# Performance work log

Measured on AMD Instinct MI355X. Metric: run time of the kernel, lower is better.

## Reference

```python
import jax, jax.numpy as jnp
import numpy as np

HIDDEN = 7168
NUM_EXPERTS = 256
TOPK = 8
NUM_GROUPS = 8
TOPK_GROUPS = 4
ROUTE_SCALE = 2.5
TOKENS = 8192


def setup_inputs() -> dict:
    key = jax.random.key(0)
    kx, kw = jax.random.split(key)
    x = jax.random.normal(kx, (TOKENS, HIDDEN), dtype=jnp.float32)
    # gate weight ~ nn.Parameter(empty) initialized here with small normal values
    weight = jax.random.normal(kw, (NUM_EXPERTS, HIDDEN), dtype=jnp.float32) * 0.02
    # bias branch is active because hidden_size == 7168
    bias = jnp.zeros((NUM_EXPERTS,), dtype=jnp.float32)
    return {"x": x, "weight": weight, "bias": bias}


def reference(x, weight, bias):
    # scores: [T, E] = sigmoid(x @ W^T)
    scores = jax.nn.sigmoid(jnp.einsum("th,eh->te", x.astype(jnp.float32), weight))
    original_scores = scores
    scores_for_choice = scores + bias  # bias is not None (hidden==7168)

    T = scores.shape[0]
    per_group = NUM_EXPERTS // NUM_GROUPS  # 32
    g = scores_for_choice.reshape(T, NUM_GROUPS, per_group)
    # bias is not None -> group score = sum of top-2 within each group
    group_scores = jax.lax.top_k(g, 2)[0].sum(axis=-1)  # [T, G]
    _, group_idx = jax.lax.top_k(group_scores, TOPK_GROUPS)  # [T, topk_groups]
    # keep-mask over groups
    keep = jnp.zeros((T, NUM_GROUPS), dtype=bool)
    keep = keep.at[jnp.arange(T)[:, None], group_idx].set(True)
    masked = jnp.where(keep[:, :, None], g, -jnp.inf).reshape(T, NUM_EXPERTS)

    _, indices = jax.lax.top_k(masked, TOPK)  # [T, topk]
    weights = jnp.take_along_axis(original_scores, indices, axis=1)
    weights = weights / (weights.sum(axis=-1, keepdims=True) + 1e-20)
    weights = weights * ROUTE_SCALE
    return weights.astype(jnp.float32), indices
```

## Files before the change

kernel.cpp:

```cpp
#include <hip/hip_runtime.h>
#include <math.h>


constexpr int T_TOK = 8192;
constexpr int HID   = 7168;
constexpr int NEXP  = 256;

constexpr int BM   = 64;
constexpr int BK   = 64;
constexpr int KSPL = 8;
constexpr int KH   = HID / KSPL;
constexpr int NIT  = KH / BK;

typedef __attribute__((ext_vector_type(8)))  _Float16 hf8;
typedef __attribute__((ext_vector_type(4)))  _Float16 hf4;
typedef __attribute__((ext_vector_type(16))) float    f32x16;

struct hl16 { _Float16 h, l; };
__device__ __forceinline__ hl16 cvt_split(float v, float scale) {
  const float s = v * scale;
  const _Float16 h = (_Float16)s;
  const _Float16 l = (_Float16)(s - (float)h);
  return {h, l};
}

__global__ __launch_bounds__(256)
void convert_w(const float* __restrict__ w, _Float16* __restrict__ wh,
               _Float16* __restrict__ wl) {
  const int gid = blockIdx.x * 256 + threadIdx.x;
  const int e = gid / (HID / 4);
  const int c = gid - e * (HID / 4);
  const float4 v = *(const float4*)(w + (size_t)gid * 4);
  const int k = 4 * c;
  const size_t o = (size_t)(k >> 3) * (NEXP * 8) + (size_t)e * 8 + (k & 7);
  hf4 h, l;
  hl16 t;
  t = cvt_split(v.x, 1024.f); h.x = t.h; l.x = t.l;
  t = cvt_split(v.y, 1024.f); h.y = t.h; l.y = t.l;
  t = cvt_split(v.z, 1024.f); h.z = t.h; l.z = t.l;
  t = cvt_split(v.w, 1024.f); h.w = t.h; l.w = t.l;
  *(hf4*)(wh + o) = h;
  *(hf4*)(wl + o) = l;
}

__global__ __launch_bounds__(512, 4)
void gemm_mfma(const float* __restrict__ x, const _Float16* __restrict__ wh,
               const _Float16* __restrict__ wl, float* __restrict__ part) {
  __shared__ __attribute__((aligned(16))) _Float16 Ah[2][BM * BK];
  __shared__ __attribute__((aligned(16))) _Float16 Al[2][BM * BK];

  const int tid = threadIdx.x;
  const int l   = tid & 63;
  const int wn  = tid >> 6;

  const int b  = blockIdx.x;
  const int kp = b & 7;
  const int t0 = (b >> 3) * BM;
  const int kb = kp * KH;

  const int sr = tid >> 3;
  const int sc = tid & 7;
  const float* xrow = x + (size_t)(t0 + sr) * HID + kb + 4 * sc;

  const int swz   = (l & 7) << 4;
  const int lrow  = l & 31;
  const int khalf = l >> 5;

  const _Float16* bhb = wh + ((size_t)(kb >> 3) + khalf) * (NEXP * 8)
                           + (size_t)(wn * 32 + lrow) * 8;
  const _Float16* blb = wl + ((size_t)(kb >> 3) + khalf) * (NEXP * 8)
                           + (size_t)(wn * 32 + lrow) * 8;

  f32x16 acc[2] = {};

  float4 xv0 = *(const float4*)(xrow);
  float4 xv1 = *(const float4*)(xrow + 32);

#pragma unroll 2
  for (int it = 0; it < NIT; ++it) {
    float4 xn0, xn1;
    const bool more = (it + 1 < NIT);
    if (more) {
      xn0 = *(const float4*)(xrow + (it + 1) * BK);
      xn1 = *(const float4*)(xrow + (it + 1) * BK + 32);
    }

    hf8 bh[4], bl[4];
    const _Float16* bhi = bhb + (size_t)it * (8 * NEXP * 8);
    const _Float16* bli = blb + (size_t)it * (8 * NEXP * 8);
#pragma unroll
    for (int ks = 0; ks < 4; ++ks) {
      bh[ks] = *(const hf8*)(bhi + ks * (2 * NEXP * 8));
      bl[ks] = *(const hf8*)(bli + ks * (2 * NEXP * 8));
    }

    _Float16* ah = &Ah[it & 1][0];
    _Float16* al = &Al[it & 1][0];
    {
      hf4 h0, h1, g0, g1;
      hl16 t;
      t = cvt_split(xv0.x, 64.f); h0.x = t.h; g0.x = t.l;
      t = cvt_split(xv0.y, 64.f); h0.y = t.h; g0.y = t.l;
      t = cvt_split(xv0.z, 64.f); h0.z = t.h; g0.z = t.l;
      t = cvt_split(xv0.w, 64.f); h0.w = t.h; g0.w = t.l;
      t = cvt_split(xv1.x, 64.f); h1.x = t.h; g1.x = t.l;
      t = cvt_split(xv1.y, 64.f); h1.y = t.h; g1.y = t.l;
      t = cvt_split(xv1.z, 64.f); h1.z = t.h; g1.z = t.l;
      t = cvt_split(xv1.w, 64.f); h1.w = t.h; g1.w = t.l;
      const int wb  = sr * (BK * 2);
      const int wsw = (sr & 7) << 4;
      *(hf4*)((char*)ah + wb + ((sc * 8)      ^ wsw)) = h0;
      *(hf4*)((char*)ah + wb + ((sc * 8 + 64) ^ wsw)) = h1;
      *(hf4*)((char*)al + wb + ((sc * 8)      ^ wsw)) = g0;
      *(hf4*)((char*)al + wb + ((sc * 8 + 64) ^ wsw)) = g1;
    }

    asm volatile("s_waitcnt lgkmcnt(0)\n\ts_barrier" ::: "memory");

#pragma unroll
    for (int ks = 0; ks < 4; ++ks) {
      const int cb = (ks * 32 + khalf * 16) ^ swz;
      const hf8 a0h = *(const hf8*)((const char*)ah + lrow * 128 + cb);
      const hf8 a1h = *(const hf8*)((const char*)ah + (32 + lrow) * 128 + cb);
      const hf8 a0l = *(const hf8*)((const char*)al + lrow * 128 + cb);
      const hf8 a1l = *(const hf8*)((const char*)al + (32 + lrow) * 128 + cb);
      acc[0] = __builtin_amdgcn_mfma_f32_32x32x16_f16(a0h, bh[ks], acc[0], 0, 0, 0);
      acc[1] = __builtin_amdgcn_mfma_f32_32x32x16_f16(a1h, bh[ks], acc[1], 0, 0, 0);
      acc[0] = __builtin_amdgcn_mfma_f32_32x32x16_f16(a0l, bh[ks], acc[0], 0, 0, 0);
      acc[1] = __builtin_amdgcn_mfma_f32_32x32x16_f16(a1l, bh[ks], acc[1], 0, 0, 0);
      acc[0] = __builtin_amdgcn_mfma_f32_32x32x16_f16(a0h, bl[ks], acc[0], 0, 0, 0);
      acc[1] = __builtin_amdgcn_mfma_f32_32x32x16_f16(a1h, bl[ks], acc[1], 0, 0, 0);
    }

    if (more) { xv0 = xn0; xv1 = xn1; }
  }

  float* pout = part + (size_t)kp * ((size_t)T_TOK * NEXP);
  const int e = wn * 32 + lrow;
#pragma unroll
  for (int mt = 0; mt < 2; ++mt)
#pragma unroll
    for (int g = 0; g < 4; ++g) {
      const int r0 = t0 + mt * 32 + 8 * g + 4 * khalf;
#pragma unroll
      for (int j = 0; j < 4; ++j)
        pout[(size_t)(r0 + j) * NEXP + e] = acc[mt][4 * g + j];
    }
}

__global__ __launch_bounds__(256)
void routing_kernel(const float* __restrict__ part,
                    const float* __restrict__ bias,
                    float* __restrict__ out) {
  const int lane = threadIdx.x & 63;
  const int t = blockIdx.x * 4 + (threadIdx.x >> 6);
  const int e_base = 4 * lane;

  float4 z = make_float4(0.f, 0.f, 0.f, 0.f);
#pragma unroll
  for (int kp = 0; kp < KSPL; ++kp) {
    float4 v = *(const float4*)(part + (size_t)kp * T_TOK * NEXP +
                                (size_t)t * NEXP + e_base);
    z.x += v.x; z.y += v.y; z.z += v.z; z.w += v.w;
  }
  constexpr float INV = 1.f / 65536.f;
  float s[4], sb[4];
  const float4 b4 = *(const float4*)(bias + e_base);
  s[0] = 1.f / (1.f + expf(-z.x * INV)); sb[0] = s[0] + b4.x;
  s[1] = 1.f / (1.f + expf(-z.y * INV)); sb[1] = s[1] + b4.y;
  s[2] = 1.f / (1.f + expf(-z.z * INV)); sb[2] = s[2] + b4.z;
  s[3] = 1.f / (1.f + expf(-z.w * INV)); sb[3] = s[3] + b4.w;

  const float Ma = fmaxf(sb[0], sb[1]), ma = fminf(sb[0], sb[1]);
  const float Mb = fmaxf(sb[2], sb[3]), mb = fminf(sb[2], sb[3]);
  float m1 = fmaxf(Ma, Mb);
  float m2 = fmaxf(fminf(Ma, Mb), fmaxf(ma, mb));
#pragma unroll
  for (int off = 1; off < 8; off <<= 1) {
    const float o1 = __shfl_xor(m1, off);
    const float o2 = __shfl_xor(m2, off);
    const float n1 = fmaxf(m1, o1);
    m2 = fmaxf(fminf(m1, o1), fmaxf(m2, o2));
    m1 = n1;
  }
  const float gsum = m1 + m2;

  float gs[8];
#pragma unroll
  for (int g = 0; g < 8; ++g) gs[g] = __shfl(gsum, g * 8);

  unsigned gmask = 0;
#pragma unroll
  for (int r = 0; r < 4; ++r) {
    int best = 0; float bv = -3.4e38f;
#pragma unroll
    for (int g = 0; g < 8; ++g) {
      const bool ok = (((gmask >> g) & 1u) == 0) && (gs[g] > bv);
      bv = ok ? gs[g] : bv;
      best = ok ? g : best;
    }
    gmask |= 1u << best;
  }

  const bool sel = (gmask >> (lane >> 3)) & 1u;
#pragma unroll
  for (int j = 0; j < 4; ++j) sb[j] = sel ? sb[j] : -3.4e38f;

  float wq[8]; float iq[8];
#pragma unroll
  for (int r = 0; r < 8; ++r) {
    float bv = sb[0]; int bi = e_base; float bs = s[0];
#pragma unroll
    for (int j = 1; j < 4; ++j) {
      const bool c = sb[j] > bv;
      bv = c ? sb[j] : bv; bi = c ? e_base + j : bi; bs = c ? s[j] : bs;
    }
#pragma unroll
    for (int off = 1; off < 64; off <<= 1) {
      const float ov = __shfl_xor(bv, off);
      const int   oi = __shfl_xor(bi, off);
      const float os = __shfl_xor(bs, off);
      const bool take = (ov > bv) || (ov == bv && oi < bi);
      bv = take ? ov : bv; bi = take ? oi : bi; bs = take ? os : bs;
    }
    wq[r] = bs; iq[r] = (float)bi;
#pragma unroll
    for (int j = 0; j < 4; ++j)
      if (e_base + j == bi) sb[j] = -3.4e38f;
  }

  float wsum = 1e-20f;
#pragma unroll
  for (int r = 0; r < 8; ++r) wsum += wq[r];
  const float scale = 2.5f / wsum;

  if (lane == 0) {
    float4* ow = (float4*)(out + (size_t)t * 8);
    ow[0] = make_float4(wq[0] * scale, wq[1] * scale, wq[2] * scale, wq[3] * scale);
    ow[1] = make_float4(wq[4] * scale, wq[5] * scale, wq[6] * scale, wq[7] * scale);
    float4* oi = (float4*)(out + (size_t)T_TOK * 8 + (size_t)t * 8);
    oi[0] = make_float4(iq[0], iq[1], iq[2], iq[3]);
    oi[1] = make_float4(iq[4], iq[5], iq[6], iq[7]);
  }
}

extern "C" void kernel_launch(void* const* d_in, const int* in_sizes, int n_in,
                              void* d_out, int out_size, void* d_ws, size_t ws_size,
                              hipStream_t stream) {
  const float* x    = (const float*)d_in[0];
  const float* w    = (const float*)d_in[1];
  const float* bias = (const float*)d_in[2];
  float* out  = (float*)d_out;
  float* part = (float*)d_ws;
  _Float16* wh = (_Float16*)((char*)d_ws + (size_t)KSPL * T_TOK * NEXP * 4);
  _Float16* wl = wh + (size_t)NEXP * HID;

  hipLaunchKernelGGL(convert_w, dim3(NEXP * HID / 4 / 256), dim3(256), 0,
                     stream, w, wh, wl);
  hipLaunchKernelGGL(gemm_mfma, dim3(1024), dim3(512), 0, stream,
                     x, wh, wl, part);
  hipLaunchKernelGGL(routing_kernel, dim3(T_TOK / 4), dim3(256), 0, stream,
                     part, bias, out);
}
```

Measured before the change: 390.7 us.

## Remap GEMM waves to 2x4 grid sharing A rows and loading B per k-step

Changes the per-wave tile from 64 tokens x 32 experts to 32 tokens x 64 experts, arranging the eight waves as a 2x4 grid. Each wave now reads half as much A from LDS per k-step but issues twice the B (weight) global loads, and those loads now happen inside the k-step loop after the barrier instead of being prefetched before it. The launch-bounds occupancy hint of 4 is dropped so the compiler has more register freedom. The risk is exposed global-load latency on B, since it is no longer fetched ahead of the MFMAs.

Result: slower. 404.3 us (+3.5%).

```diff
diff --git a/kernel.cpp b/kernel.cpp
--- a/kernel.cpp
+++ b/kernel.cpp
@@ -43,7 +43,7 @@
   *(hf4*)(wl + o) = l;
 }
 
-__global__ __launch_bounds__(512, 4)
+__global__ __launch_bounds__(512)
 void gemm_mfma(const float* __restrict__ x, const _Float16* __restrict__ wh,
                const _Float16* __restrict__ wl, float* __restrict__ part) {
   __shared__ __attribute__((aligned(16))) _Float16 Ah[2][BM * BK];
@@ -51,7 +51,9 @@
 
   const int tid = threadIdx.x;
   const int l   = tid & 63;
-  const int wn  = tid >> 6;
+  const int wv  = tid >> 6;
+  const int wm  = wv & 1;
+  const int wq  = wv >> 1;
 
   const int b  = blockIdx.x;
   const int kp = b & 7;
@@ -65,11 +67,12 @@
   const int swz   = (l & 7) << 4;
   const int lrow  = l & 31;
   const int khalf = l >> 5;
+  const int arow  = (wm * 32 + lrow) * 128;
 
   const _Float16* bhb = wh + ((size_t)(kb >> 3) + khalf) * (NEXP * 8)
-                           + (size_t)(wn * 32 + lrow) * 8;
+                           + (size_t)(wq * 64 + lrow) * 8;
   const _Float16* blb = wl + ((size_t)(kb >> 3) + khalf) * (NEXP * 8)
-                           + (size_t)(wn * 32 + lrow) * 8;
+                           + (size_t)(wq * 64 + lrow) * 8;
 
   f32x16 acc[2] = {};
 
@@ -85,14 +88,8 @@
       xn1 = *(const float4*)(xrow + (it + 1) * BK + 32);
     }
 
-    hf8 bh[4], bl[4];
     const _Float16* bhi = bhb + (size_t)it * (8 * NEXP * 8);
     const _Float16* bli = blb + (size_t)it * (8 * NEXP * 8);
-#pragma unroll
-    for (int ks = 0; ks < 4; ++ks) {
-      bh[ks] = *(const hf8*)(bhi + ks * (2 * NEXP * 8));
-      bl[ks] = *(const hf8*)(bli + ks * (2 * NEXP * 8));
-    }
 
     _Float16* ah = &Ah[it & 1][0];
     _Float16* al = &Al[it & 1][0];
@@ -119,32 +116,36 @@
 
 #pragma unroll
     for (int ks = 0; ks < 4; ++ks) {
+      const _Float16* bks_h = bhi + ks * (2 * NEXP * 8);
+      const _Float16* bks_l = bli + ks * (2 * NEXP * 8);
+      const hf8 bh0 = *(const hf8*)(bks_h);
+      const hf8 bh1 = *(const hf8*)(bks_h + 256);
+      const hf8 bl0 = *(const hf8*)(bks_l);
+      const hf8 bl1 = *(const hf8*)(bks_l + 256);
       const int cb = (ks * 32 + khalf * 16) ^ swz;
-      const hf8 a0h = *(const hf8*)((const char*)ah + lrow * 128 + cb);
-      const hf8 a1h = *(const hf8*)((const char*)ah + (32 + lrow) * 128 + cb);
-      const hf8 a0l = *(const hf8*)((const char*)al + lrow * 128 + cb);
-      const hf8 a1l = *(const hf8*)((const char*)al + (32 + lrow) * 128 + cb);
-      acc[0] = __builtin_amdgcn_mfma_f32_32x32x16_f16(a0h, bh[ks], acc[0], 0, 0, 0);
-      acc[1] = __builtin_amdgcn_mfma_f32_32x32x16_f16(a1h, bh[ks], acc[1], 0, 0, 0);
-      acc[0] = __builtin_amdgcn_mfma_f32_32x32x16_f16(a0l, bh[ks], acc[0], 0, 0, 0);
-      acc[1] = __builtin_amdgcn_mfma_f32_32x32x16_f16(a1l, bh[ks], acc[1], 0, 0, 0);
-      acc[0] = __builtin_amdgcn_mfma_f32_32x32x16_f16(a0h, bl[ks], acc[0], 0, 0, 0);
-      acc[1] = __builtin_amdgcn_mfma_f32_32x32x16_f16(a1h, bl[ks], acc[1], 0, 0, 0);
+      const hf8 a_h = *(const hf8*)((const char*)ah + arow + cb);
+      const hf8 a_l = *(const hf8*)((const char*)al + arow + cb);
+      acc[0] = __builtin_amdgcn_mfma_f32_32x32x16_f16(a_h, bh0, acc[0], 0, 0, 0);
+      acc[1] = __builtin_amdgcn_mfma_f32_32x32x16_f16(a_h, bh1, acc[1], 0, 0, 0);
+      acc[0] = __builtin_amdgcn_mfma_f32_32x32x16_f16(a_l, bh0, acc[0], 0, 0, 0);
+      acc[1] = __builtin_amdgcn_mfma_f32_32x32x16_f16(a_l, bh1, acc[1], 0, 0, 0);
+      acc[0] = __builtin_amdgcn_mfma_f32_32x32x16_f16(a_h, bl0, acc[0], 0, 0, 0);
+      acc[1] = __builtin_amdgcn_mfma_f32_32x32x16_f16(a_h, bl1, acc[1], 0, 0, 0);
     }
 
     if (more) { xv0 = xn0; xv1 = xn1; }
   }
 
   float* pout = part + (size_t)kp * ((size_t)T_TOK * NEXP);
-  const int e = wn * 32 + lrow;
-#pragma unroll
-  for (int mt = 0; mt < 2; ++mt)
+  const int e = wq * 64 + lrow;
+#pragma unroll
+  for (int es = 0; es < 2; ++es)
 #pragma unroll
     for (int g = 0; g < 4; ++g) {
-      const int r0 = t0 + mt * 32 + 8 * g + 4 * khalf;
+      const int r0 = t0 + wm * 32 + 8 * g + 4 * khalf;
 #pragma unroll
       for (int j = 0; j < 4; ++j)
-        pout[(size_t)(r0 + j) * NEXP + e] = acc[mt][4 * g + j];
+        pout[(size_t)(r0 + j) * NEXP + e + es * 32] = acc[es][4 * g + j];
     }
 }
 
```
